# Performance work log

Measured on AMD Instinct MI355X. Metric: run time of the kernel, lower is better.

## Reference

```python
import jax, jax.numpy as jnp
import numpy as np

B, S, E, H, NL = 64, 256, 1024, 16, 2
D = E // H          # head dim = 64
FF = 4 * E          # 4096
EPS = 1e-5
MASKED = -10000.0   # masked_bias buffer value


def layer_norm(x, g, b):
    m = jnp.mean(x, axis=-1, keepdims=True)
    v = jnp.mean(jnp.square(x - m), axis=-1, keepdims=True)
    return (x - m) * jax.lax.rsqrt(v + EPS) * g + b


def setup_inputs() -> dict:
    key = jax.random.key(0)
    ks = jax.random.split(key, 8)
    s = 0.02
    return {
        "sentence_hidden": jax.random.normal(ks[0], (B, S, E), dtype=jnp.float32),
        "wpe": jax.random.normal(ks[1], (256, E), dtype=jnp.float32) * s,
        "ln1_g": jnp.ones((NL, E), jnp.float32),
        "ln1_b": jnp.zeros((NL, E), jnp.float32),
        "attn_w": jax.random.normal(ks[2], (NL, E, 3 * E), dtype=jnp.float32) * s,
        "attn_b": jnp.zeros((NL, 3 * E), jnp.float32),
        "attn_proj_w": jax.random.normal(ks[3], (NL, E, E), dtype=jnp.float32) * s,
        "attn_proj_b": jnp.zeros((NL, E), jnp.float32),
        "ln2_g": jnp.ones((NL, E), jnp.float32),
        "ln2_b": jnp.zeros((NL, E), jnp.float32),
        "fc_w": jax.random.normal(ks[4], (NL, E, FF), dtype=jnp.float32) * s,
        "fc_b": jnp.zeros((NL, FF), jnp.float32),
        "mlp_proj_w": jax.random.normal(ks[5], (NL, FF, E), dtype=jnp.float32) * s,
        "mlp_proj_b": jnp.zeros((NL, E), jnp.float32),
        "lnf_g": jnp.ones((E,), jnp.float32),
        "lnf_b": jnp.zeros((E,), jnp.float32),
    }


def reference(sentence_hidden, wpe, ln1_g, ln1_b, attn_w, attn_b, attn_proj_w,
              attn_proj_b, ln2_g, ln2_b, fc_w, fc_b, mlp_proj_w, mlp_proj_b,
              lnf_g, lnf_b):
    # position embeddings: positions 0..S-1 (wpe has 256 rows, S == 256)
    h = sentence_hidden + wpe[:S][None, :, :]
    causal = jnp.tril(jnp.ones((S, S), dtype=bool))  # [S,S]
    scale = 1.0 / np.sqrt(D)
    for i in range(NL):
        # --- attention ---
        x = layer_norm(h, ln1_g[i], ln1_b[i])
        qkv = x @ attn_w[i] + attn_b[i]                    # [B,S,3E]
        q, k, v = jnp.split(qkv, 3, axis=-1)
        q = q.reshape(B, S, H, D).transpose(0, 2, 1, 3)    # [B,H,S,D]
        k = k.reshape(B, S, H, D).transpose(0, 2, 1, 3)
        v = v.reshape(B, S, H, D).transpose(0, 2, 1, 3)
        w = jnp.einsum("bhqd,bhkd->bhqk", q, k) * scale    # [B,H,S,S]
        w = jnp.where(causal, w, jnp.asarray(MASKED, w.dtype))
        w = jax.nn.softmax(w, axis=-1)
        a = jnp.einsum("bhqk,bhkd->bhqd", w, v)            # [B,H,S,D]
        a = a.transpose(0, 2, 1, 3).reshape(B, S, E)
        a = a @ attn_proj_w[i] + attn_proj_b[i]
        h = h + a
        # --- MLP ---
        x = layer_norm(h, ln2_g[i], ln2_b[i])
        m = jax.nn.gelu(x @ fc_w[i] + fc_b[i], approximate=True)  # gelu_new
        m = m @ mlp_proj_w[i] + mlp_proj_b[i]
        h = h + m
    h = layer_norm(h, lnf_g, lnf_b)
    loss = jnp.mean(jnp.square(h[0, :-1, :] - sentence_hidden[0, 1:, :]))
    return (h, loss)
```

## Files before the change

### kernel.cpp

```cpp
#include <hip/hip_runtime.h>
#include <cstdint>
#include <cstddef>


typedef __attribute__((ext_vector_type(4))) float f32x4;
typedef __attribute__((ext_vector_type(16))) float f32x16;
typedef __attribute__((ext_vector_type(8))) __bf16 bf16x8;
typedef __attribute__((ext_vector_type(4))) unsigned int u32x4;
typedef __attribute__((ext_vector_type(8))) unsigned short u16x8;
typedef __attribute__((ext_vector_type(4))) unsigned short u16x4;

__device__ __forceinline__ unsigned short f2bf(float x) {
  unsigned int u = __builtin_bit_cast(unsigned int, x);
  u += 0x7fffu + ((u >> 16) & 1u);
  return (unsigned short)(u >> 16);
}
__device__ __forceinline__ float gelu_new(float x) {
  float u = 0.7978845608028654f * (x + 0.044715f * x * x * x);
  return x * __builtin_amdgcn_rcpf(1.0f + __expf(-2.0f * u));
}
__device__ __forceinline__ unsigned int cvtpk(float lo, float hi) {
  unsigned int r;
  asm("v_cvt_pk_bf16_f32 %0, %1, %2" : "=v"(r) : "v"(lo), "v"(hi));
  return r;
}
__device__ __forceinline__ void plswap(unsigned int& a, unsigned int& b) {
  asm("v_permlane32_swap_b32 %0, %1" : "+v"(a), "+v"(b));
}

__global__ __launch_bounds__(256) void transpose_bf16(
    const float* __restrict__ W, unsigned short* __restrict__ Wt, int K, int N) {
  __shared__ float tile[32][33];
  const int n0 = blockIdx.x * 32, k0 = blockIdx.y * 32;
  const int tx = threadIdx.x, ty = threadIdx.y;
#pragma unroll
  for (int j = 0; j < 32; j += 8)
    tile[ty + j][tx] = W[(size_t)(k0 + ty + j) * N + n0 + tx];
  __syncthreads();
#pragma unroll
  for (int j = 0; j < 32; j += 8)
    Wt[(size_t)(n0 + ty + j) * K + k0 + tx] = f2bf(tile[tx][ty + j]);
}

template <int OUTF32>
__global__ __launch_bounds__(256) void ln4_kernel(
    const float* __restrict__ hin, const float* __restrict__ g,
    const float* __restrict__ bb, void* __restrict__ outp) {
  const int lane = threadIdx.x & 63;
  const int row = blockIdx.x * 4 + (threadIdx.x >> 6);
  const f32x4* src = (const f32x4*)(hin + (size_t)row * 1024);
  f32x4 v[4];
#pragma unroll
  for (int j = 0; j < 4; ++j) v[j] = src[j * 64 + lane];
  float s = 0.f, sq = 0.f;
#pragma unroll
  for (int j = 0; j < 4; ++j) {
    s += v[j].x + v[j].y + v[j].z + v[j].w;
    sq += v[j].x * v[j].x + v[j].y * v[j].y + v[j].z * v[j].z + v[j].w * v[j].w;
  }
#pragma unroll
  for (int off = 32; off; off >>= 1) {
    s += __shfl_xor(s, off, 64);
    sq += __shfl_xor(sq, off, 64);
  }
  const float mean = s * (1.0f / 1024.0f);
  const float var = sq * (1.0f / 1024.0f) - mean * mean;
  const float rs = rsqrtf(var + 1e-5f);
#pragma unroll
  for (int j = 0; j < 4; ++j) {
    const f32x4 gv = ((const f32x4*)g)[j * 64 + lane];
    const f32x4 bv = ((const f32x4*)bb)[j * 64 + lane];
    float y0 = (v[j].x - mean) * rs * gv.x + bv.x;
    float y1 = (v[j].y - mean) * rs * gv.y + bv.y;
    float y2 = (v[j].z - mean) * rs * gv.z + bv.z;
    float y3 = (v[j].w - mean) * rs * gv.w + bv.w;
    if (OUTF32) {
      f32x4 o; o.x = y0; o.y = y1; o.z = y2; o.w = y3;
      ((f32x4*)outp)[(size_t)row * 256 + j * 64 + lane] = o;
    } else {
      u16x4 pk;
      pk.x = f2bf(y0); pk.y = f2bf(y1); pk.z = f2bf(y2); pk.w = f2bf(y3);
      ((u16x4*)outp)[(size_t)row * 256 + j * 64 + lane] = pk;
    }
  }
}

__global__ __launch_bounds__(256) void ln4_wpe_kernel(
    const float* __restrict__ sent, const float* __restrict__ wpe,
    const float* __restrict__ g, const float* __restrict__ bb,
    float* __restrict__ h, unsigned short* __restrict__ xb) {
  const int lane = threadIdx.x & 63;
  const int row = blockIdx.x * 4 + (threadIdx.x >> 6);
  const int sp = row & 255;
  const f32x4* src = (const f32x4*)(sent + (size_t)row * 1024);
  const f32x4* wp = (const f32x4*)(wpe + (size_t)sp * 1024);
  f32x4* hp = (f32x4*)(h + (size_t)row * 1024);
  f32x4 v[4];
#pragma unroll
  for (int j = 0; j < 4; ++j) {
    v[j] = src[j * 64 + lane] + wp[j * 64 + lane];
    hp[j * 64 + lane] = v[j];
  }
  float s = 0.f, sq = 0.f;
#pragma unroll
  for (int j = 0; j < 4; ++j) {
    s += v[j].x + v[j].y + v[j].z + v[j].w;
    sq += v[j].x * v[j].x + v[j].y * v[j].y + v[j].z * v[j].z + v[j].w * v[j].w;
  }
#pragma unroll
  for (int off = 32; off; off >>= 1) {
    s += __shfl_xor(s, off, 64);
    sq += __shfl_xor(sq, off, 64);
  }
  const float mean = s * (1.0f / 1024.0f);
  const float var = sq * (1.0f / 1024.0f) - mean * mean;
  const float rs = rsqrtf(var + 1e-5f);
#pragma unroll
  for (int j = 0; j < 4; ++j) {
    const f32x4 gv = ((const f32x4*)g)[j * 64 + lane];
    const f32x4 bv = ((const f32x4*)bb)[j * 64 + lane];
    u16x4 pk;
    pk.x = f2bf((v[j].x - mean) * rs * gv.x + bv.x);
    pk.y = f2bf((v[j].y - mean) * rs * gv.y + bv.y);
    pk.z = f2bf((v[j].z - mean) * rs * gv.z + bv.z);
    pk.w = f2bf((v[j].w - mean) * rs * gv.w + bv.w);
    ((u16x4*)xb)[(size_t)row * 256 + j * 64 + lane] = pk;
  }
}

template <int EPI>
__global__ __launch_bounds__(512, 2) void gemmp(
    const unsigned short* __restrict__ A, const unsigned short* __restrict__ Bt,
    const float* __restrict__ bias, unsigned short* __restrict__ Cb,
    float* __restrict__ Hres, int N, int K, int gx, int gy) {
  constexpr int A_E = 16384;
  constexpr int BUF_E = A_E + 16384;
  __shared__ alignas(16) unsigned short smem[2 * BUF_E];

  const int nwg = gx * gy;
  const int dd = blockIdx.x;
  const int wrk = (dd & 7) * (nwg >> 3) + (dd >> 3);
  const int cid = wrk >> 4;
  const int cin = wrk & 15;
  const int cpr = gx >> 2;
  const int cby = cid / cpr;
  const int cbx = cid - cby * cpr;
  const int bx = cbx * 4 + (cin & 3);
  const int by = cby * 4 + (cin >> 2);
  const int row0 = by * 256, col0 = bx * 256;

  const int t = threadIdx.x;
  const int wid = t >> 6, l = t & 63;
  const int wm = wid >> 2, wn = wid & 3;
  const int fr = l & 15, q4 = l >> 4;

  const int cx0 = (q4 ^ (fr & 7)) * 8;
  const int cx1 = ((4 + q4) ^ (fr & 7)) * 8;
  const int b_r0 = (wn * 64 + fr) * 64;
  auto a_slot = [&](int m) -> int { return (wm * 128 + m * 16 + fr) * 64; };

  const int lrow = l >> 3;
  const int scol = ((l & 7) ^ (lrow & 7)) * 8;

  auto stB = [&](int tt, int win) {
    const unsigned short* s =
        Bt + (size_t)(col0 + win * 8 + lrow) * K + tt * 64 + scol;
    __builtin_amdgcn_global_load_lds(
        (const __attribute__((address_space(1))) void*)s,
        (__attribute__((address_space(3))) void*)(smem + (tt & 1) * BUF_E + A_E + win * 512),
        16, 0, 0);
  };
  auto stA = [&](int tt, int win) {
    const unsigned short* s =
        A + (size_t)(row0 + win * 8 + lrow) * K + tt * 64 + scol;
    __builtin_amdgcn_global_load_lds(
        (const __attribute__((address_space(1))) void*)s,
        (__attribute__((address_space(3))) void*)(smem + (tt & 1) * BUF_E + win * 512),
        16, 0, 0);
  };
  auto stageB_set = [&](int tt) {
    stB(tt, 2 * wid); stB(tt, 2 * wid + 1);
    stB(tt, 16 + 2 * wid); stB(tt, 16 + 2 * wid + 1);
  };
  auto stageA_set = [&](int tt) {
    const int i0 = 2 * wid, i1 = 2 * wid + 1;
    stA(tt, i0 < 8 ? i0 : 8 + i0);
    stA(tt, i1 < 8 ? i1 : 8 + i1);
    stA(tt, i0 < 8 ? 8 + i0 : 16 + i0);
    stA(tt, i1 < 8 ? 8 + i1 : 16 + i1);
  };

  const int nt = K >> 6;

  stageB_set(0);
  stageA_set(0);
  asm volatile("s_waitcnt vmcnt(2)" ::: "memory");
  __builtin_amdgcn_s_barrier();
  asm volatile("" ::: "memory");

  f32x4 acc[8][4];
#pragma unroll
  for (int m = 0; m < 8; ++m)
#pragma unroll
    for (int n = 0; n < 4; ++n) {
      acc[m][n].x = 0.f; acc[m][n].y = 0.f; acc[m][n].z = 0.f; acc[m][n].w = 0.f;
    }

  for (int tc = 0; tc < nt; ++tc) {
    const unsigned short* Ab = smem + (tc & 1) * BUF_E;
    const unsigned short* Bb = Ab + A_E;
    const bool pf = (tc + 1) < nt;

    bf16x8 b0[4], b1[4], a0[4], a1[4];
#pragma unroll
    for (int n = 0; n < 4; ++n) b0[n] = *(const bf16x8*)(Bb + b_r0 + n * 1024 + cx0);
#pragma unroll
    for (int m = 0; m < 4; ++m) a0[m] = *(const bf16x8*)(Ab + a_slot(m) + cx0);
#pragma unroll
    for (int n = 0; n < 4; ++n) b1[n] = *(const bf16x8*)(Bb + b_r0 + n * 1024 + cx1);
#pragma unroll
    for (int m = 0; m < 4; ++m) a1[m] = *(const bf16x8*)(Ab + a_slot(m) + cx1);

    if (pf) { stageB_set(tc + 1); stageA_set(tc + 1); }

    __builtin_amdgcn_s_setprio(1);
#pragma unroll
    for (int m = 0; m < 4; ++m)
#pragma unroll
      for (int n = 0; n < 4; ++n)
        acc[m][n] = __builtin_amdgcn_mfma_f32_16x16x32_bf16(a0[m], b0[n], acc[m][n], 0, 0, 0);
    __builtin_amdgcn_s_setprio(0);

    __builtin_amdgcn_s_setprio(1);
#pragma unroll
    for (int m = 0; m < 4; ++m)
#pragma unroll
      for (int n = 0; n < 4; ++n)
        acc[m][n] = __builtin_amdgcn_mfma_f32_16x16x32_bf16(a1[m], b1[n], acc[m][n], 0, 0, 0);
    __builtin_amdgcn_s_setprio(0);

    if (pf) asm volatile("s_waitcnt vmcnt(8)" ::: "memory");
    else    asm volatile("s_waitcnt vmcnt(0)" ::: "memory");
    __builtin_amdgcn_s_barrier();
    asm volatile("" ::: "memory");

    bf16x8 h0[4], h1[4];
#pragma unroll
    for (int m = 0; m < 4; ++m) h0[m] = *(const bf16x8*)(Ab + a_slot(4 + m) + cx0);
#pragma unroll
    for (int m = 0; m < 4; ++m) h1[m] = *(const bf16x8*)(Ab + a_slot(4 + m) + cx1);

    __builtin_amdgcn_s_setprio(1);
#pragma unroll
    for (int m = 0; m < 4; ++m)
#pragma unroll
      for (int n = 0; n < 4; ++n)
        acc[4 + m][n] = __builtin_amdgcn_mfma_f32_16x16x32_bf16(h0[m], b0[n], acc[4 + m][n], 0, 0, 0);
    __builtin_amdgcn_s_setprio(0);
    __builtin_amdgcn_s_setprio(1);
#pragma unroll
    for (int m = 0; m < 4; ++m)
#pragma unroll
      for (int n = 0; n < 4; ++n)
        acc[4 + m][n] = __builtin_amdgcn_mfma_f32_16x16x32_bf16(h1[m], b1[n], acc[4 + m][n], 0, 0, 0);
    __builtin_amdgcn_s_setprio(0);

    if (pf) asm volatile("s_waitcnt vmcnt(2)" ::: "memory");
    else    asm volatile("s_waitcnt vmcnt(0)" ::: "memory");
    __builtin_amdgcn_s_barrier();
    asm volatile("" ::: "memory");
  }

  if constexpr (EPI == 2) {
#pragma unroll
    for (int n = 0; n < 4; ++n) {
      const int col = col0 + wn * 64 + n * 16 + fr;
      const float bi = bias[col];
#pragma unroll
      for (int m = 0; m < 8; ++m)
#pragma unroll
        for (int e = 0; e < 4; ++e) {
          const int row = row0 + wm * 128 + m * 16 + q4 * 4 + e;
          Hres[(size_t)row * N + col] += acc[m][n][e] + bi;
        }
    }
  } else {
    char* wreg = (char*)smem + wid * 9216;
    float bi[4];
#pragma unroll
    for (int n = 0; n < 4; ++n) bi[n] = bias[col0 + wn * 64 + n * 16 + fr];
#pragma unroll
    for (int half = 0; half < 2; ++half) {
#pragma unroll
      for (int m = 0; m < 4; ++m)
#pragma unroll
        for (int n = 0; n < 4; ++n)
#pragma unroll
          for (int e = 0; e < 4; ++e) {
            float v = acc[half * 4 + m][n][e] + bi[n];
            if (EPI == 1) v = gelu_new(v);
            *(unsigned short*)(wreg + (m * 16 + q4 * 4 + e) * 144 +
                               (n * 16 + fr) * 2) = f2bf(v);
          }
#pragma unroll
      for (int rb = 0; rb < 8; ++rb) {
        const int rowl = rb * 8 + (l >> 3);
        u16x8 vv = *(const u16x8*)(wreg + rowl * 144 + (l & 7) * 16);
        const int rg = row0 + wm * 128 + half * 64 + rowl;
        *(u16x8*)(Cb + (size_t)rg * N + col0 + wn * 64 + (l & 7) * 8) = vv;
      }
    }
  }
}

__global__ __launch_bounds__(256) void attn_mfma(
    const unsigned short* __restrict__ qkv, unsigned short* __restrict__ aout,
    int b0) {
  __shared__ alignas(16) unsigned short Klds[256 * 64];
  __shared__ alignas(16) unsigned short Vt[64 * 256];
  const int bh = blockIdx.x;
  const int bl = bh >> 4, hd = bh & 15;
  const size_t base = (size_t)bl * 256 * 3072 + (size_t)hd * 64;
  const int t = threadIdx.x;
  const int w = t >> 6, l = t & 63;
  const int lq = l & 31, hl = l >> 5;

#pragma unroll
  for (int i = 0; i < 8; ++i) {
    const int r = i * 32 + (t >> 3);
    const int c = t & 7;
    u16x8 kv = *(const u16x8*)(qkv + base + (size_t)r * 3072 + 1024 + c * 8);
    *(u16x8*)(Klds + r * 64 + ((c ^ (r & 7)) * 8)) = kv;
    u16x8 vv = *(const u16x8*)(qkv + base + (size_t)r * 3072 + 2048 + c * 8);
#pragma unroll
    for (int j = 0; j < 8; ++j) {
      const int d = c * 8 + j;
      Vt[d * 256 + (((r >> 3) ^ (d & 31)) * 8) + (r & 7)] = vv[j];
    }
  }

  const int q0 = w * 64;
  bf16x8 qf[2][4];
#pragma unroll
  for (int n = 0; n < 2; ++n)
#pragma unroll
    for (int d16 = 0; d16 < 4; ++d16)
      qf[n][d16] = *(const bf16x8*)(qkv + base +
          (size_t)(q0 + n * 32 + lq) * 3072 + d16 * 16 + hl * 8);
  __syncthreads();

  const float cs = 0.125f * 1.44269504088896f;
  f32x16 O[2][2];
#pragma unroll
  for (int m = 0; m < 2; ++m)
#pragma unroll
    for (int n = 0; n < 2; ++n)
#pragma unroll
      for (int e = 0; e < 16; ++e) O[m][n][e] = 0.f;
  float mrun[2] = {-3.0e38f, -3.0e38f};
  float lrun[2] = {0.f, 0.f};

  const int ktmax = (q0 + 63) >> 5;
  for (int kt = 0; kt <= ktmax; ++kt) {
    bf16x8 kf[4];
    const int krow = kt * 32 + lq;
#pragma unroll
    for (int d16 = 0; d16 < 4; ++d16) {
      const int chunk = (d16 * 2 + hl) ^ (krow & 7);
      kf[d16] = *(const bf16x8*)(Klds + krow * 64 + chunk * 8);
    }
    const int nlo = (kt * 32 > q0 + 31) ? 1 : 0;
    bf16x8 pfrag[2][2];
#pragma unroll
    for (int n = 0; n < 2; ++n) {
      if (n < nlo) continue;
      f32x16 s;
#pragma unroll
      for (int e = 0; e < 16; ++e) s[e] = 0.f;
#pragma unroll
      for (int d16 = 0; d16 < 4; ++d16)
        s = __builtin_amdgcn_mfma_f32_32x32x16_bf16(kf[d16], qf[n][d16], s, 0, 0, 0);
      const int qg = q0 + n * 32 + lq;
      float sv[16];
#pragma unroll
      for (int r = 0; r < 16; ++r) {
        const int kg = kt * 32 + (r & 3) + 8 * (r >> 2) + 4 * hl;
        const float x = s[r] * cs;
        sv[r] = (kg > qg) ? -3.0e38f : x;
      }
      float pmax = sv[0];
#pragma unroll
      for (int r = 1; r < 16; ++r) pmax = fmaxf(pmax, sv[r]);
      pmax = fmaxf(pmax, __shfl_xor(pmax, 32, 64));
      const float nm = fmaxf(mrun[n], pmax);
      const float alpha = exp2f(mrun[n] - nm);
      mrun[n] = nm;
      float psum = 0.f;
#pragma unroll
      for (int r = 0; r < 16; ++r) {
        sv[r] = exp2f(sv[r] - nm);
        psum += sv[r];
      }
      psum += __shfl_xor(psum, 32, 64);
      lrun[n] = lrun[n] * alpha + psum;
#pragma unroll
      for (int m = 0; m < 2; ++m)
#pragma unroll
        for (int e = 0; e < 16; ++e) O[m][n][e] *= alpha;
#pragma unroll
      for (int h = 0; h < 2; ++h) {
        unsigned int a0 = cvtpk(sv[h * 8 + 0], sv[h * 8 + 1]);
        unsigned int a1 = cvtpk(sv[h * 8 + 2], sv[h * 8 + 3]);
        unsigned int c0 = cvtpk(sv[h * 8 + 4], sv[h * 8 + 5]);
        unsigned int c1 = cvtpk(sv[h * 8 + 6], sv[h * 8 + 7]);
        plswap(a0, c0);
        plswap(a1, c1);
        u32x4 fw; fw.x = a0; fw.y = a1; fw.z = c0; fw.w = c1;
        pfrag[n][h] = __builtin_bit_cast(bf16x8, fw);
      }
    }
#pragma unroll
    for (int m = 0; m < 2; ++m)
#pragma unroll
      for (int h = 0; h < 2; ++h) {
        const int dd = m * 32 + lq;
        const int chunk = (kt * 4 + h * 2 + hl) ^ (dd & 31);
        bf16x8 vf = *(const bf16x8*)(Vt + dd * 256 + chunk * 8);
#pragma unroll
        for (int n = 0; n < 2; ++n)
          if (n >= nlo)
            O[m][n] = __builtin_amdgcn_mfma_f32_32x32x16_bf16(vf, pfrag[n][h], O[m][n], 0, 0, 0);
      }
  }

#pragma unroll
  for (int n = 0; n < 2; ++n) {
    const float inv = 1.0f / lrun[n];
    const size_t row = (size_t)(b0 + bl) * 256 + q0 + n * 32 + lq;
#pragma unroll
    for (int m = 0; m < 2; ++m) {
#pragma unroll
      for (int qd = 0; qd < 4; ++qd) {
        u16x4 pk;
#pragma unroll
        for (int e = 0; e < 4; ++e) pk[e] = f2bf(O[m][n][qd * 4 + e] * inv);
        *(u16x4*)(aout + row * 1024 + hd * 64 + m * 32 + qd * 8 + hl * 4) = pk;
      }
    }
  }
}

__device__ __forceinline__ float block_reduce_sum256(float v) {
#pragma unroll
  for (int off = 32; off; off >>= 1) v += __shfl_xor(v, off, 64);
  __shared__ float red[4];
  const int t = threadIdx.x;
  if ((t & 63) == 0) red[t >> 6] = v;
  __syncthreads();
  return red[0] + red[1] + red[2] + red[3];
}

__global__ __launch_bounds__(256) void loss_partial(
    const float* __restrict__ hf, const float* __restrict__ sent,
    float* __restrict__ part) {
  const int s = blockIdx.x, t = threadIdx.x;
  f32x4 a = ((const f32x4*)(hf + (size_t)s * 1024))[t];
  f32x4 b = ((const f32x4*)(sent + (size_t)(s + 1) * 1024))[t];
  f32x4 d = a - b;
  float v = d.x * d.x + d.y * d.y + d.z * d.z + d.w * d.w;
  float tot = block_reduce_sum256(v);
  if (t == 0) part[s] = tot;
}

__global__ __launch_bounds__(256) void loss_final(
    const float* __restrict__ part, float* __restrict__ out) {
  const int t = threadIdx.x;
  float v = (t < 255) ? part[t] : 0.f;
  float s = block_reduce_sum256(v);
  if (t == 0) out[0] = s * (1.0f / (255.0f * 1024.0f));
}

constexpr size_t C_X     = 0;
constexpr size_t C_QKV   = 33554432;
constexpr size_t C_WQKV  = C_QKV + 67108864;
constexpr size_t C_WPROJ = C_WQKV + 6291456;
constexpr size_t C_WFC   = C_WPROJ + 2097152;
constexpr size_t C_WMLP  = C_WFC + 8388608;
constexpr size_t C_PART  = C_WMLP + 8388608;

constexpr size_t F_X     = 0;
constexpr size_t F_U     = 33554432;
constexpr size_t F_WQKV  = F_U + 134217728;
constexpr size_t F_WPROJ = F_WQKV + 6291456;
constexpr size_t F_WFC   = F_WPROJ + 2097152;
constexpr size_t F_WMLP  = F_WFC + 8388608;
constexpr size_t F_PART  = F_WMLP + 8388608;
constexpr size_t F_NEED  = F_PART + 4096;

extern "C" void kernel_launch(void* const* d_in, const int* in_sizes, int n_in,
                              void* d_out, int out_size, void* d_ws, size_t ws_size,
                              hipStream_t stream) {
  (void)in_sizes; (void)n_in; (void)out_size;
  const float* sent    = (const float*)d_in[0];
  const float* wpe     = (const float*)d_in[1];
  const float* ln1_g   = (const float*)d_in[2];
  const float* ln1_b   = (const float*)d_in[3];
  const float* attn_w  = (const float*)d_in[4];
  const float* attn_b  = (const float*)d_in[5];
  const float* attn_pw = (const float*)d_in[6];
  const float* attn_pb = (const float*)d_in[7];
  const float* ln2_g   = (const float*)d_in[8];
  const float* ln2_b   = (const float*)d_in[9];
  const float* fc_w    = (const float*)d_in[10];
  const float* fc_b    = (const float*)d_in[11];
  const float* mlp_w   = (const float*)d_in[12];
  const float* mlp_b   = (const float*)d_in[13];
  const float* lnf_g   = (const float*)d_in[14];
  const float* lnf_b   = (const float*)d_in[15];
  float* out_h = (float*)d_out;
  float* h = out_h;

  char* ws = (char*)d_ws;
  const bool fullm = ws_size >= F_NEED;

  unsigned short* xb    = (unsigned short*)(ws + (fullm ? F_X : C_X));
  unsigned short* ub    = (unsigned short*)(ws + (fullm ? F_U : C_QKV));
  unsigned short* wqkv  = (unsigned short*)(ws + (fullm ? F_WQKV : C_WQKV));
  unsigned short* wproj = (unsigned short*)(ws + (fullm ? F_WPROJ : C_WPROJ));
  unsigned short* wfc   = (unsigned short*)(ws + (fullm ? F_WFC : C_WFC));
  unsigned short* wmlp  = (unsigned short*)(ws + (fullm ? F_WMLP : C_WMLP));
  float* part           = (float*)(ws + (fullm ? F_PART : C_PART));

  const dim3 tb(32, 8, 1);
  for (int i = 0; i < 2; ++i) {
    transpose_bf16<<<dim3(96, 32), tb, 0, stream>>>(
        attn_w + (size_t)i * 1024 * 3072, wqkv, 1024, 3072);
    transpose_bf16<<<dim3(32, 32), tb, 0, stream>>>(
        attn_pw + (size_t)i * 1024 * 1024, wproj, 1024, 1024);
    transpose_bf16<<<dim3(128, 32), tb, 0, stream>>>(
        fc_w + (size_t)i * 1024 * 4096, wfc, 1024, 4096);
    transpose_bf16<<<dim3(32, 128), tb, 0, stream>>>(
        mlp_w + (size_t)i * 4096 * 1024, wmlp, 4096, 1024);

    if (i == 0)
      ln4_wpe_kernel<<<4096, 256, 0, stream>>>(sent, wpe, ln1_g, ln1_b, h, xb);
    else
      ln4_kernel<0><<<4096, 256, 0, stream>>>(h, ln1_g + i * 1024, ln1_b + i * 1024, xb);

    if (fullm) {
      gemmp<0><<<768, 512, 0, stream>>>(
          xb, wqkv, attn_b + i * 3072, ub, nullptr, 3072, 1024, 12, 64);
      attn_mfma<<<1024, 256, 0, stream>>>(ub, xb, 0);
    } else {
      for (int c = 0; c < 2; ++c) {
        const size_t r0 = (size_t)c * 8192;
        gemmp<0><<<384, 512, 0, stream>>>(
            xb + r0 * 1024, wqkv, attn_b + i * 3072, ub, nullptr, 3072, 1024, 12, 32);
        attn_mfma<<<512, 256, 0, stream>>>(ub, xb, c * 32);
      }
    }
    gemmp<2><<<256, 512, 0, stream>>>(
        xb, wproj, attn_pb + i * 1024, nullptr, h, 1024, 1024, 4, 64);

    ln4_kernel<0><<<4096, 256, 0, stream>>>(h, ln2_g + i * 1024, ln2_b + i * 1024, xb);
    if (fullm) {
      gemmp<1><<<1024, 512, 0, stream>>>(
          xb, wfc, fc_b + i * 4096, ub, nullptr, 4096, 1024, 16, 64);
      gemmp<2><<<256, 512, 0, stream>>>(
          ub, wmlp, mlp_b + i * 1024, nullptr, h, 1024, 4096, 4, 64);
    } else {
      for (int c = 0; c < 2; ++c) {
        const size_t r0 = (size_t)c * 8192;
        gemmp<1><<<512, 512, 0, stream>>>(
            xb + r0 * 1024, wfc, fc_b + i * 4096, ub, nullptr, 4096, 1024, 16, 32);
        gemmp<2><<<128, 512, 0, stream>>>(
            ub, wmlp, mlp_b + i * 1024, nullptr, h + r0 * 1024, 1024, 4096, 4, 32);
      }
    }
  }

  ln4_kernel<1><<<4096, 256, 0, stream>>>(h, lnf_g, lnf_b, out_h);
  loss_partial<<<255, 256, 0, stream>>>(out_h, sent, part);
  loss_final<<<1, 256, 0, stream>>>(part, out_h + 16777216);
}
```

Measured before the change: 1.153 ms.

## Store residual stream in bf16 and stagger A/B prefetch in GEMM loop

The residual stream h moves from fp32 in the output buffer to a bf16 workspace buffer when enough workspace is available. The LayerNorm kernels read bf16 input, and the residual-add GEMM epilogue does a vectorized bf16 read-modify-write through the shared-memory staging path instead of scalar fp32 atomic-free adds. This halves residual traffic and turns strided scalar stores into coalesced ones, at the cost of rounding error accumulating in the residual. The GEMM main loop also issues the A-tile prefetch after the first MFMA batch rather than together with the B prefetch, and the low-memory chunked fallback path is removed.

```diff
diff --git a/kernel.cpp b/kernel.cpp
--- a/kernel.cpp
+++ b/kernel.cpp
@@ -15,6 +15,9 @@
   u += 0x7fffu + ((u >> 16) & 1u);
   return (unsigned short)(u >> 16);
 }
+__device__ __forceinline__ float b2f(unsigned short x) {
+  return __builtin_bit_cast(float, (unsigned int)x << 16);
+}
 __device__ __forceinline__ float gelu_new(float x) {
   float u = 0.7978845608028654f * (x + 0.044715f * x * x * x);
   return x * __builtin_amdgcn_rcpf(1.0f + __expf(-2.0f * u));
@@ -42,16 +45,25 @@
     Wt[(size_t)(n0 + ty + j) * K + k0 + tx] = f2bf(tile[tx][ty + j]);
 }
 
-template <int OUTF32>
+template <int INBF, int OUTF32>
 __global__ __launch_bounds__(256) void ln4_kernel(
-    const float* __restrict__ hin, const float* __restrict__ g,
+    const void* __restrict__ hin, const float* __restrict__ g,
     const float* __restrict__ bb, void* __restrict__ outp) {
   const int lane = threadIdx.x & 63;
   const int row = blockIdx.x * 4 + (threadIdx.x >> 6);
-  const f32x4* src = (const f32x4*)(hin + (size_t)row * 1024);
   f32x4 v[4];
-#pragma unroll
-  for (int j = 0; j < 4; ++j) v[j] = src[j * 64 + lane];
+  if (INBF) {
+    const u16x4* src = (const u16x4*)hin + (size_t)row * 256;
+#pragma unroll
+    for (int j = 0; j < 4; ++j) {
+      u16x4 w = src[j * 64 + lane];
+      v[j].x = b2f(w.x); v[j].y = b2f(w.y); v[j].z = b2f(w.z); v[j].w = b2f(w.w);
+    }
+  } else {
+    const f32x4* src = (const f32x4*)hin + (size_t)row * 256;
+#pragma unroll
+    for (int j = 0; j < 4; ++j) v[j] = src[j * 64 + lane];
+  }
   float s = 0.f, sq = 0.f;
 #pragma unroll
   for (int j = 0; j < 4; ++j) {
@@ -85,21 +97,29 @@
   }
 }
 
+template <int HBF>
 __global__ __launch_bounds__(256) void ln4_wpe_kernel(
     const float* __restrict__ sent, const float* __restrict__ wpe,
     const float* __restrict__ g, const float* __restrict__ bb,
-    float* __restrict__ h, unsigned short* __restrict__ xb) {
+    void* __restrict__ h, unsigned short* __restrict__ xb) {
   const int lane = threadIdx.x & 63;
   const int row = blockIdx.x * 4 + (threadIdx.x >> 6);
   const int sp = row & 255;
   const f32x4* src = (const f32x4*)(sent + (size_t)row * 1024);
   const f32x4* wp = (const f32x4*)(wpe + (size_t)sp * 1024);
-  f32x4* hp = (f32x4*)(h + (size_t)row * 1024);
   f32x4 v[4];
 #pragma unroll
   for (int j = 0; j < 4; ++j) {
     v[j] = src[j * 64 + lane] + wp[j * 64 + lane];
-    hp[j * 64 + lane] = v[j];
+    if (HBF) {
+      u16x4 pk;
+      pk.x = f2bf(v[j].x); pk.y = f2bf(v[j].y);
+      pk.z = f2bf(v[j].z); pk.w = f2bf(v[j].w);
+      ((u16x4*)h)[(size_t)row * 256 + j * 64 + lane] = pk;
+      v[j].x = b2f(pk.x); v[j].y = b2f(pk.y); v[j].z = b2f(pk.z); v[j].w = b2f(pk.w);
+    } else {
+      ((f32x4*)h)[(size_t)row * 256 + j * 64 + lane] = v[j];
+    }
   }
   float s = 0.f, sq = 0.f;
 #pragma unroll
@@ -128,11 +148,11 @@
   }
 }
 
-template <int EPI>
+template <int EPI, int HBF>
 __global__ __launch_bounds__(512, 2) void gemmp(
     const unsigned short* __restrict__ A, const unsigned short* __restrict__ Bt,
     const float* __restrict__ bias, unsigned short* __restrict__ Cb,
-    float* __restrict__ Hres, int N, int K, int gx, int gy) {
+    void* __restrict__ Hres, int N, int K, int gx, int gy) {
   constexpr int A_E = 16384;
   constexpr int BUF_E = A_E + 16384;
   __shared__ alignas(16) unsigned short smem[2 * BUF_E];
@@ -221,7 +241,7 @@
 #pragma unroll
     for (int m = 0; m < 4; ++m) a1[m] = *(const bf16x8*)(Ab + a_slot(m) + cx1);
 
-    if (pf) { stageB_set(tc + 1); stageA_set(tc + 1); }
+    if (pf) stageB_set(tc + 1);
 
     __builtin_amdgcn_s_setprio(1);
 #pragma unroll
@@ -230,6 +250,8 @@
       for (int n = 0; n < 4; ++n)
         acc[m][n] = __builtin_amdgcn_mfma_f32_16x16x32_bf16(a0[m], b0[n], acc[m][n], 0, 0, 0);
     __builtin_amdgcn_s_setprio(0);
+
+    if (pf) stageA_set(tc + 1);
 
     __builtin_amdgcn_s_setprio(1);
 #pragma unroll
@@ -271,7 +293,8 @@
     asm volatile("" ::: "memory");
   }
 
-  if constexpr (EPI == 2) {
+  if constexpr (EPI == 2 && HBF == 0) {
+    float* Hf = (float*)Hres;
 #pragma unroll
     for (int n = 0; n < 4; ++n) {
       const int col = col0 + wn * 64 + n * 16 + fr;
@@ -281,10 +304,11 @@
 #pragma unroll
         for (int e = 0; e < 4; ++e) {
           const int row = row0 + wm * 128 + m * 16 + q4 * 4 + e;
-          Hres[(size_t)row * N + col] += acc[m][n][e] + bi;
+          Hf[(size_t)row * N + col] += acc[m][n][e] + bi;
         }
     }
   } else {
+    unsigned short* Hb = (unsigned short*)Hres;
     char* wreg = (char*)smem + wid * 9216;
     float bi[4];
 #pragma unroll
@@ -307,7 +331,17 @@
         const int rowl = rb * 8 + (l >> 3);
         u16x8 vv = *(const u16x8*)(wreg + rowl * 144 + (l & 7) * 16);
         const int rg = row0 + wm * 128 + half * 64 + rowl;
-        *(u16x8*)(Cb + (size_t)rg * N + col0 + wn * 64 + (l & 7) * 8) = vv;
+        unsigned short* dst =
+            (EPI == 2 ? Hb : Cb) + (size_t)rg * N + col0 + wn * 64 + (l & 7) * 8;
+        if (EPI == 2) {
+          u16x8 hv = *(const u16x8*)dst;
+          u16x8 o;
+#pragma unroll
+          for (int e = 0; e < 8; ++e) o[e] = f2bf(b2f(hv[e]) + b2f(vv[e]));
+          *(u16x8*)dst = o;
+        } else {
+          *(u16x8*)dst = vv;
+        }
       }
     }
   }
@@ -480,14 +514,6 @@
   if (t == 0) out[0] = s * (1.0f / (255.0f * 1024.0f));
 }
 
-constexpr size_t C_X     = 0;
-constexpr size_t C_QKV   = 33554432;
-constexpr size_t C_WQKV  = C_QKV + 67108864;
-constexpr size_t C_WPROJ = C_WQKV + 6291456;
-constexpr size_t C_WFC   = C_WPROJ + 2097152;
-constexpr size_t C_WMLP  = C_WFC + 8388608;
-constexpr size_t C_PART  = C_WMLP + 8388608;
-
 constexpr size_t F_X     = 0;
 constexpr size_t F_U     = 33554432;
 constexpr size_t F_WQKV  = F_U + 134217728;
@@ -495,7 +521,16 @@
 constexpr size_t F_WFC   = F_WPROJ + 2097152;
 constexpr size_t F_WMLP  = F_WFC + 8388608;
 constexpr size_t F_PART  = F_WMLP + 8388608;
-constexpr size_t F_NEED  = F_PART + 4096;
+
+constexpr size_t G_X     = 0;
+constexpr size_t G_H     = 33554432;
+constexpr size_t G_U     = G_H + 33554432;
+constexpr size_t G_WQKV  = G_U + 134217728;
+constexpr size_t G_WPROJ = G_WQKV + 6291456;
+constexpr size_t G_WFC   = G_WPROJ + 2097152;
+constexpr size_t G_WMLP  = G_WFC + 8388608;
+constexpr size_t G_PART  = G_WMLP + 8388608;
+constexpr size_t G_NEED  = G_PART + 4096;
 
 extern "C" void kernel_launch(void* const* d_in, const int* in_sizes, int n_in,
                               void* d_out, int out_size, void* d_ws, size_t ws_size,
@@ -518,18 +553,20 @@
   const float* lnf_g   = (const float*)d_in[14];
   const float* lnf_b   = (const float*)d_in[15];
   float* out_h = (float*)d_out;
-  float* h = out_h;
 
   char* ws = (char*)d_ws;
-  const bool fullm = ws_size >= F_NEED;
-
-  unsigned short* xb    = (unsigned short*)(ws + (fullm ? F_X : C_X));
-  unsigned short* ub    = (unsigned short*)(ws + (fullm ? F_U : C_QKV));
-  unsigned short* wqkv  = (unsigned short*)(ws + (fullm ? F_WQKV : C_WQKV));
-  unsigned short* wproj = (unsigned short*)(ws + (fullm ? F_WPROJ : C_WPROJ));
-  unsigned short* wfc   = (unsigned short*)(ws + (fullm ? F_WFC : C_WFC));
-  unsigned short* wmlp  = (unsigned short*)(ws + (fullm ? F_WMLP : C_WMLP));
-  float* part           = (float*)(ws + (fullm ? F_PART : C_PART));
+  const bool t2 = ws_size >= G_NEED;
+
+  unsigned short* xb    = (unsigned short*)(ws + (t2 ? G_X : F_X));
+  unsigned short* hb    = (unsigned short*)(ws + G_H);
+  unsigned short* ub    = (unsigned short*)(ws + (t2 ? G_U : F_U));
+  unsigned short* wqkv  = (unsigned short*)(ws + (t2 ? G_WQKV : F_WQKV));
+  unsigned short* wproj = (unsigned short*)(ws + (t2 ? G_WPROJ : F_WPROJ));
+  unsigned short* wfc   = (unsigned short*)(ws + (t2 ? G_WFC : F_WFC));
+  unsigned short* wmlp  = (unsigned short*)(ws + (t2 ? G_WMLP : F_WMLP));
+  float* part           = (float*)(ws + (t2 ? G_PART : F_PART));
+
+  void* h = t2 ? (void*)hb : (void*)out_h;
 
   const dim3 tb(32, 8, 1);
   for (int i = 0; i < 2; ++i) {
@@ -542,44 +579,41 @@
     transpose_bf16<<<dim3(32, 128), tb, 0, stream>>>(
         mlp_w + (size_t)i * 4096 * 1024, wmlp, 4096, 1024);
 
-    if (i == 0)
-      ln4_wpe_kernel<<<4096, 256, 0, stream>>>(sent, wpe, ln1_g, ln1_b, h, xb);
+    if (i == 0) {
+      if (t2) ln4_wpe_kernel<1><<<4096, 256, 0, stream>>>(sent, wpe, ln1_g, ln1_b, h, xb);
+      else    ln4_wpe_kernel<0><<<4096, 256, 0, stream>>>(sent, wpe, ln1_g, ln1_b, h, xb);
+    } else {
+      if (t2) ln4_kernel<1, 0><<<4096, 256, 0, stream>>>(h, ln1_g + i * 1024, ln1_b + i * 1024, xb);
+      else    ln4_kernel<0, 0><<<4096, 256, 0, stream>>>(h, ln1_g + i * 1024, ln1_b + i * 1024, xb);
+    }
+
+    gemmp<0, 0><<<768, 512, 0, stream>>>(
+        xb, wqkv, attn_b + i * 3072, ub, nullptr, 3072, 1024, 12, 64);
+    attn_mfma<<<1024, 256, 0, stream>>>(ub, xb, 0);
+
+    if (t2)
+      gemmp<2, 1><<<256, 512, 0, stream>>>(
+          xb, wproj, attn_pb + i * 1024, nullptr, h, 1024, 1024, 4, 64);
     else
-      ln4_kernel<0><<<4096, 256, 0, stream>>>(h, ln1_g + i * 1024, ln1_b + i * 1024, xb);
-
-    if (fullm) {
-      gemmp<0><<<768, 512, 0, stream>>>(
-          xb, wqkv, attn_b + i * 3072, ub, nullptr, 3072, 1024, 12, 64);
-      attn_mfma<<<1024, 256, 0, stream>>>(ub, xb, 0);
-    } else {
-      for (int c = 0; c < 2; ++c) {
-        const size_t r0 = (size_t)c * 8192;
-        gemmp<0><<<384, 512, 0, stream>>>(
-            xb + r0 * 1024, wqkv, attn_b + i * 3072, ub, nullptr, 3072, 1024, 12, 32);
-        attn_mfma<<<512, 256, 0, stream>>>(ub, xb, c * 32);
-      }
-    }
-    gemmp<2><<<256, 512, 0, stream>>>(
-        xb, wproj, attn_pb + i * 1024, nullptr, h, 1024, 1024, 4, 64);
-
-    ln4_kernel<0><<<4096, 256, 0, stream>>>(h, ln2_g + i * 1024, ln2_b + i * 1024, xb);
-    if (fullm) {
-      gemmp<1><<<1024, 512, 0, stream>>>(
-          xb, wfc, fc_b + i * 4096, ub, nullptr, 4096, 1024, 16, 64);
-      gemmp<2><<<256, 512, 0, stream>>>(
+      gemmp<2, 0><<<256, 512, 0, stream>>>(
+          xb, wproj, attn_pb + i * 1024, nullptr, h, 1024, 1024, 4, 64);
+
+    if (t2) ln4_kernel<1, 0><<<4096, 256, 0, stream>>>(h, ln2_g + i * 1024, ln2_b + i * 1024, xb);
+    else    ln4_kernel<0, 0><<<4096, 256, 0, stream>>>(h, ln2_g + i * 1024, ln2_b + i * 1024, xb);
+
+    gemmp<1, 0><<<1024, 512, 0, stream>>>(
+        xb, wfc, fc_b + i * 4096, ub, nullptr, 4096, 1024, 16, 64);
+
+    if (t2)
+      gemmp<2, 1><<<256, 512, 0, stream>>>(
           ub, wmlp, mlp_b + i * 1024, nullptr, h, 1024, 4096, 4, 64);
-    } else {
-      for (int c = 0; c < 2; ++c) {
-        const size_t r0 = (size_t)c * 8192;
-        gemmp<1><<<512, 512, 0, stream>>>(
-            xb + r0 * 1024, wfc, fc_b + i * 4096, ub, nullptr, 4096, 1024, 16, 32);
-        gemmp<2><<<128, 512, 0, stream>>>(
-            ub, wmlp, mlp_b + i * 1024, nullptr, h + r0 * 1024, 1024, 4096, 4, 32);
-      }
-    }
-  }
-
-  ln4_kernel<1><<<4096, 256, 0, stream>>>(h, lnf_g, lnf_b, out_h);
+    else
+      gemmp<2, 0><<<256, 512, 0, stream>>>(
+          ub, wmlp, mlp_b + i * 1024, nullptr, h, 1024, 4096, 4, 64);
+  }
+
+  if (t2) ln4_kernel<1, 1><<<4096, 256, 0, stream>>>(h, lnf_g, lnf_b, out_h);
+  else    ln4_kernel<0, 1><<<4096, 256, 0, stream>>>(h, lnf_g, lnf_b, out_h);
   loss_partial<<<255, 256, 0, stream>>>(out_h, sent, part);
   loss_final<<<1, 256, 0, stream>>>(part, out_h + 16777216);
 }
```

Result: faster. 1.048 ms (-9.1%).
